# Performance work log

Hardware: AMD Instinct MI355X
Metric: run time of the kernel (lower is better)

## Reference

```python
import jax, jax.numpy as jnp
import numpy as np

B, N, D_IN, D_OUT = 2, 2048, 2048, 2048
H, G = 16, 4            # num_heads, n_kv_groups
HD = D_OUT // H         # head_dim = 128
REP = H // G            # query heads per kv head = 4


def setup_inputs() -> dict:
    key = jax.random.key(0)
    ks = jax.random.split(key, 6)
    s = lambda fan_in: 1.0 / np.sqrt(fan_in)
    return {
        "x": jax.random.normal(ks[0], (B, N, D_IN), jnp.float32),
        "Wq": jax.random.normal(ks[1], (D_IN, D_OUT), jnp.float32) * s(D_IN),
        "Wk": jax.random.normal(ks[2], (D_IN, G * HD), jnp.float32) * s(D_IN),
        "Wv": jax.random.normal(ks[3], (D_IN, G * HD), jnp.float32) * s(D_IN),
        "Wo": jax.random.normal(ks[4], (D_OUT, D_OUT), jnp.float32) * s(D_OUT),
        "bo": jnp.zeros((D_OUT,), jnp.float32),
    }


def reference(x, Wq, Wk, Wv, Wo, bo):
    b, n, _ = x.shape
    # projections
    q = (x @ Wq).reshape(b, n, G, REP, HD)   # query heads grouped: h = g*REP + r
    k = (x @ Wk).reshape(b, n, G, HD)
    v = (x @ Wv).reshape(b, n, G, HD)
    # grouped attention scores; KV broadcast over REP instead of repeat_kv
    scores = jnp.einsum('bqgrd,bkgd->bgrqk', q, k)  # [b,G,REP,N,N]
    causal = jnp.tril(jnp.ones((n, n), bool))       # allowed positions
    scores = jnp.where(causal, scores, -jnp.inf)
    w = jax.nn.softmax(scores / np.float32(np.sqrt(HD)), axis=-1)
    ctx = jnp.einsum('bgrqk,bkgd->bqgrd', w, v).reshape(b, n, D_OUT)
    return ctx @ Wo + bo
```

## Files before the change

kernel.cpp:

```cpp
#include <hip/hip_runtime.h>
#include <stdint.h>

typedef __attribute__((ext_vector_type(8))) __bf16 bf16x8;
typedef __attribute__((ext_vector_type(4))) float f32x4;
typedef __attribute__((ext_vector_type(4))) short short4v;

static constexpr int SEQ  = 2048;
static constexpr int DQKV = 3072;
static constexpr int HD   = 128;

__device__ __forceinline__ short f2bf(float f) {
  unsigned u = __builtin_bit_cast(unsigned, f);
  u += 0x7fffu + ((u >> 16) & 1u);
  return (short)(u >> 16);
}

__device__ __forceinline__ unsigned pack2(float a, float b) {
  return (unsigned)(unsigned short)f2bf(a) | ((unsigned)(unsigned short)f2bf(b) << 16);
}

__device__ __forceinline__ void gl_lds16(const void* g, void* l) {
  __builtin_amdgcn_global_load_lds(
      (const __attribute__((address_space(1))) void*)g,
      (__attribute__((address_space(3))) void*)l, 16, 0, 0);
}

__global__ __launch_bounds__(256)
void prep_kernel(const float* __restrict__ x, const float* __restrict__ Wq,
                 const float* __restrict__ Wk, const float* __restrict__ Wv,
                 const float* __restrict__ Wo,
                 short* __restrict__ xb, short* __restrict__ WqkvT,
                 short* __restrict__ WoT) {
  int blk = blockIdx.x, tid = threadIdx.x;
  if (blk < 8192) {
    int i = blk * 256 + tid;
    float4 v = reinterpret_cast<const float4*>(x)[i];
    short4v o;
    o[0] = f2bf(v.x); o[1] = f2bf(v.y); o[2] = f2bf(v.z); o[3] = f2bf(v.w);
    *reinterpret_cast<short4v*>(xb + (size_t)i * 4) = o;
    return;
  }
  blk -= 8192;
  __shared__ float tile[32][33];
  const float* in; short* out; int C, bx, by;
  if (blk < 4096)      { in = Wq; out = WqkvT;                     C = 2048; bx = blk & 63; by = blk >> 6; }
  else if (blk < 5120) { int t = blk - 4096; in = Wk; out = WqkvT + (size_t)2048 * 2048; C = 512; bx = t & 15; by = t >> 4; }
  else if (blk < 6144) { int t = blk - 5120; in = Wv; out = WqkvT + (size_t)2560 * 2048; C = 512; bx = t & 15; by = t >> 4; }
  else                 { int t = blk - 6144; in = Wo; out = WoT;   C = 2048; bx = t & 63; by = t >> 6; }
  const int R = 2048;
  int c0 = bx * 32, r0 = by * 32, tx = tid & 31, ty = tid >> 5;
  for (int i = 0; i < 4; i++)
    tile[ty + i * 8][tx] = in[(size_t)(r0 + ty + i * 8) * C + c0 + tx];
  __syncthreads();
  for (int i = 0; i < 4; i++)
    out[(size_t)(c0 + ty + i * 8) * R + r0 + tx] = f2bf(tile[tx][ty + i * 8]);
}

template <int MODE>
__device__ __forceinline__
void gemm_body(const short* __restrict__ A, const short* __restrict__ BT,
               void* __restrict__ Cout, const float* __restrict__ bias,
               short* __restrict__ vTout, int N, int K, int GX, float qscale) {
  __shared__ __align__(16) short As[4096];
  __shared__ __align__(16) short Bs[4096];
  const int tid = threadIdx.x, lane = tid & 63, w = tid >> 6;
  const int l15 = lane & 15, quad = lane >> 4, q8 = quad * 8;
  const int bid = blockIdx.x, stripe = GX >> 3;
  const int bx = (bid & 7) * stripe + ((bid >> 3) % stripe);
  const int by = (bid >> 3) / stripe;
  const int row0 = by * 128, col0 = bx * 128;
  const int wm = (w >> 1) * 64, wn = (w & 1) * 64;
  f32x4 acc[4][4] = {};
  const short* ga0 = A  + (size_t)(row0 + w * 16 + (lane >> 2)) * K + (lane & 3) * 8;
  const short* gb0 = BT + (size_t)(col0 + w * 16 + (lane >> 2)) * K + (lane & 3) * 8;
  for (int kt = 0; kt < K; kt += 32) {
    gl_lds16(ga0 + kt,                   As + w * 512);
    gl_lds16(ga0 + (size_t)64 * K + kt,  As + 2048 + w * 512);
    gl_lds16(gb0 + kt,                   Bs + w * 512);
    gl_lds16(gb0 + (size_t)64 * K + kt,  Bs + 2048 + w * 512);
    __syncthreads();
    bf16x8 af[4], bfr[4];
    for (int i = 0; i < 4; i++)
      af[i] = *reinterpret_cast<const bf16x8*>(As + (wm + i * 16 + l15) * 32 + q8);
    for (int j = 0; j < 4; j++)
      bfr[j] = *reinterpret_cast<const bf16x8*>(Bs + (wn + j * 16 + l15) * 32 + q8);
    for (int i = 0; i < 4; i++)
      for (int j = 0; j < 4; j++)
        acc[i][j] = __builtin_amdgcn_mfma_f32_16x16x32_bf16(af[i], bfr[j], acc[i][j], 0, 0, 0);
    __syncthreads();
  }
  if (MODE == 1) {
    float* C = (float*)Cout;
    for (int j = 0; j < 4; j++) {
      int col = col0 + wn + j * 16 + l15;
      float bv = bias[col];
      for (int i = 0; i < 4; i++)
        for (int r = 0; r < 4; r++)
          C[(size_t)(row0 + wm + i * 16 + quad * 4 + r) * N + col] = acc[i][j][r] + bv;
    }
  } else {
    short* C = (short*)Cout;
    for (int j = 0; j < 4; j++) {
      int col = col0 + wn + j * 16 + l15;
      float sc = (col < 2048) ? qscale : 1.0f;
      for (int i = 0; i < 4; i++)
        for (int r = 0; r < 4; r++)
          C[(size_t)(row0 + wm + i * 16 + quad * 4 + r) * N + col] = f2bf(acc[i][j][r] * sc);
    }
    if (col0 >= 2560) {
      for (int j = 0; j < 4; j++) {
        int vc = col0 + wn + j * 16 + l15 - 2560;
        for (int i = 0; i < 4; i++) {
          int rowg = row0 + wm + i * 16 + quad * 4;
          int b = rowg >> 11, n = rowg & 2047;
          uint2 dd = make_uint2(
              (unsigned)(unsigned short)f2bf(acc[i][j][0]) |
                  ((unsigned)(unsigned short)f2bf(acc[i][j][1]) << 16),
              (unsigned)(unsigned short)f2bf(acc[i][j][2]) |
                  ((unsigned)(unsigned short)f2bf(acc[i][j][3]) << 16));
          *reinterpret_cast<uint2*>(vTout + (size_t)(b * 512 + vc) * 2048 + n) = dd;
        }
      }
    }
  }
}

__global__ __launch_bounds__(256)
void qkv_gemm_kernel(const short* __restrict__ A, const short* __restrict__ BT,
                     short* __restrict__ C, short* __restrict__ vT, float qscale) {
  gemm_body<0>(A, BT, C, nullptr, vT, 3072, 2048, 24, qscale);
}

__global__ __launch_bounds__(256)
void out_gemm_kernel(const short* __restrict__ A, const short* __restrict__ BT,
                     float* __restrict__ C, const float* __restrict__ bias) {
  gemm_body<1>(A, BT, C, bias, nullptr, 2048, 2048, 16, 1.0f);
}

__global__ __launch_bounds__(256, 2)
void attn_kernel(const short* __restrict__ qkv, const short* __restrict__ vT,
                 short* __restrict__ ctx) {
  __shared__ __align__(16) short Ks[16384];
  __shared__ __align__(16) short Vs[16384];
  __shared__ __align__(16) short Ps[4608];
  const int tid = threadIdx.x, lane = tid & 63, w = tid >> 6;
  const int l15 = lane & 15, quad = lane >> 4, q8 = quad * 8;
  const int idx = blockIdx.x;
  const int qt = 31 - (idx >> 5);
  const int h = (idx >> 1) & 15, b = idx & 1, g = h >> 2;

  bf16x8 qf[4];
  {
    const short* gq = qkv + (size_t)(b * SEQ + qt * 64 + w * 16 + l15) * DQKV + h * HD + q8;
    for (int ds = 0; ds < 4; ds++)
      qf[ds] = *reinterpret_cast<const bf16x8*>(gq + ds * 32);
  }
  bf16x8 ones;
  for (int i = 0; i < 8; i++) ones[i] = __builtin_bit_cast(__bf16, (short)0x3F80);

  f32x4 acco[8] = {};
  f32x4 accl = {};

  auto stage = [&](int buf, int kt) {
    const short* gk = qkv + (size_t)(b * SEQ + kt * 64 + w * 16 + (lane >> 2)) * DQKV +
                      2048 + g * HD + (lane & 3) * 8;
    for (int ks = 0; ks < 4; ks++)
      gl_lds16(gk + ks * 32, Ks + buf * 8192 + ks * 2048 + w * 512);
    for (int c = 0; c < 2; c++)
      for (int ih = 0; ih < 2; ih++)
        gl_lds16(vT + (size_t)(b * 512 + g * HD + ih * 64 + w * 16 + (lane >> 2)) * SEQ +
                     kt * 64 + c * 32 + (lane & 3) * 8,
                 Vs + buf * 8192 + c * 4096 + ih * 2048 + w * 512);
  };

  stage(0, 0);
  for (int kt = 0; kt <= qt; kt++) {
    const int cur = kt & 1;
    __syncthreads();
    if (kt < qt) stage(cur ^ 1, kt + 1);

    const short* Kb = Ks + cur * 8192;
    const short* Vb = Vs + cur * 8192;

    f32x4 accs[4] = {};
    for (int ds = 0; ds < 4; ds++)
      for (int j = 0; j < 4; j++) {
        bf16x8 kf = *reinterpret_cast<const bf16x8*>(Kb + ds * 2048 + (j * 16 + l15) * 32 + q8);
        accs[j] = __builtin_amdgcn_mfma_f32_16x16x32_bf16(kf, qf[ds], accs[j], 0, 0, 0);
      }

    if (kt == qt) {
      const int q = w * 16 + l15;
      for (int j = 0; j < 4; j++)
        for (int r = 0; r < 4; r++)
          if (j * 16 + quad * 4 + r > q) accs[j][r] = -1e38f;
    }

    for (int j = 0; j < 4; j++) {
      float p0 = exp2f(accs[j][0]), p1 = exp2f(accs[j][1]);
      float p2 = exp2f(accs[j][2]), p3 = exp2f(accs[j][3]);
      unsigned u0 = __builtin_bit_cast(unsigned, p0), u1 = __builtin_bit_cast(unsigned, p1);
      unsigned u2 = __builtin_bit_cast(unsigned, p2), u3 = __builtin_bit_cast(unsigned, p3);
      uint2 dd = make_uint2((u0 >> 16) | (u1 & 0xffff0000u),
                            (u2 >> 16) | (u3 & 0xffff0000u));
      *reinterpret_cast<uint2*>(Ps + w * 1152 + l15 * 72 + j * 16 + quad * 4) = dd;
    }
    asm volatile("s_waitcnt lgkmcnt(0)" ::: "memory");

    for (int c = 0; c < 2; c++) {
      bf16x8 pf = *reinterpret_cast<const bf16x8*>(Ps + w * 1152 + l15 * 72 + c * 32 + q8);
      accl = __builtin_amdgcn_mfma_f32_16x16x32_bf16(ones, pf, accl, 0, 0, 0);
      for (int nt = 0; nt < 8; nt++) {
        bf16x8 vf = *reinterpret_cast<const bf16x8*>(Vb + c * 4096 + (nt * 16 + l15) * 32 + q8);
        acco[nt] = __builtin_amdgcn_mfma_f32_16x16x32_bf16(vf, pf, acco[nt], 0, 0, 0);
      }
    }
  }

  const float invl = 1.f / accl[0];
  const size_t row = (size_t)(b * SEQ + qt * 64 + w * 16 + l15);
  for (int nt = 0; nt < 8; nt++) {
    uint2 dd = make_uint2(pack2(acco[nt][0] * invl, acco[nt][1] * invl),
                          pack2(acco[nt][2] * invl, acco[nt][3] * invl));
    *reinterpret_cast<uint2*>(ctx + row * 2048 + h * HD + nt * 16 + quad * 4) = dd;
  }
}

extern "C" void kernel_launch(void* const* d_in, const int* in_sizes, int n_in,
                              void* d_out, int out_size, void* d_ws, size_t ws_size,
                              hipStream_t stream) {
  const float* x  = (const float*)d_in[0];
  const float* Wq = (const float*)d_in[1];
  const float* Wk = (const float*)d_in[2];
  const float* Wv = (const float*)d_in[3];
  const float* Wo = (const float*)d_in[4];
  const float* bo = (const float*)d_in[5];
  float* out = (float*)d_out;

  const float sc2 = 0.08838834764831845f * 1.4426950408889634f;

  short* xb    = (short*)d_ws;
  short* WqkvT = xb    + (size_t)4096 * 2048;
  short* WoT   = WqkvT + (size_t)3072 * 2048;
  short* qkv   = WoT   + (size_t)2048 * 2048;
  short* vT    = qkv   + (size_t)4096 * 3072;
  short* ctx   = vT    + (size_t)1024 * 2048;

  prep_kernel<<<dim3(18432), dim3(256), 0, stream>>>(x, Wq, Wk, Wv, Wo, xb, WqkvT, WoT);
  qkv_gemm_kernel<<<dim3(768), dim3(256), 0, stream>>>(xb, WqkvT, qkv, vT, sc2);
  attn_kernel<<<dim3(1024), dim3(256), 0, stream>>>(qkv, vT, ctx);
  out_gemm_kernel<<<dim3(512), dim3(256), 0, stream>>>(ctx, WoT, out, bo);
}
```

Before: 314.3 us.

## Split V transpose into separate kernel and use plain 2D GEMM grid

Replaces the swizzled 1D block mapping in the GEMMs with a plain 2D grid and removes the V-transpose write from the QKV GEMM epilogue, adding a standalone tiled transpose kernel instead. This simplifies the GEMM epilogue and removes the strided vT stores from it. In exchange it adds a kernel launch, re-reads V from global memory, and gives up the L2-locality grouping of the previous block order.

After: 305.6 us. 2.8% less time.

```diff
diff --git a/kernel.cpp b/kernel.cpp
--- a/kernel.cpp
+++ b/kernel.cpp
@@ -56,19 +56,28 @@
     out[(size_t)(c0 + ty + i * 8) * R + r0 + tx] = f2bf(tile[tx][ty + i * 8]);
 }
 
-template <int MODE>
-__device__ __forceinline__
-void gemm_body(const short* __restrict__ A, const short* __restrict__ BT,
-               void* __restrict__ Cout, const float* __restrict__ bias,
-               short* __restrict__ vTout, int N, int K, int GX, float qscale) {
+__global__ __launch_bounds__(256) void transpose_v_kernel(const short* __restrict__ qkv,
+                                                          short* __restrict__ vT) {
+  __shared__ short tile[32][33];
+  int n0 = blockIdx.x * 32, c0 = blockIdx.y * 32, b = blockIdx.z;
+  int tx = threadIdx.x & 31, ty = threadIdx.x >> 5;
+  for (int i = 0; i < 4; i++)
+    tile[ty + i * 8][tx] = qkv[(size_t)(b * SEQ + n0 + ty + i * 8) * DQKV + 2560 + c0 + tx];
+  __syncthreads();
+  for (int i = 0; i < 4; i++)
+    vT[(size_t)(b * 512 + c0 + ty + i * 8) * SEQ + n0 + tx] = tile[tx][ty + i * 8];
+}
+
+template <int F32OUT>
+__global__ __launch_bounds__(256)
+void gemm_bt_kernel(const short* __restrict__ A, const short* __restrict__ BT,
+                    void* __restrict__ Cout, const float* __restrict__ bias,
+                    int M, int N, int K, int qcols, float qscale) {
   __shared__ __align__(16) short As[4096];
   __shared__ __align__(16) short Bs[4096];
   const int tid = threadIdx.x, lane = tid & 63, w = tid >> 6;
   const int l15 = lane & 15, quad = lane >> 4, q8 = quad * 8;
-  const int bid = blockIdx.x, stripe = GX >> 3;
-  const int bx = (bid & 7) * stripe + ((bid >> 3) % stripe);
-  const int by = (bid >> 3) / stripe;
-  const int row0 = by * 128, col0 = bx * 128;
+  const int row0 = blockIdx.y * 128, col0 = blockIdx.x * 128;
   const int wm = (w >> 1) * 64, wn = (w & 1) * 64;
   f32x4 acc[4][4] = {};
   const short* ga0 = A  + (size_t)(row0 + w * 16 + (lane >> 2)) * K + (lane & 3) * 8;
@@ -89,7 +98,7 @@
         acc[i][j] = __builtin_amdgcn_mfma_f32_16x16x32_bf16(af[i], bfr[j], acc[i][j], 0, 0, 0);
     __syncthreads();
   }
-  if (MODE == 1) {
+  if (F32OUT) {
     float* C = (float*)Cout;
     for (int j = 0; j < 4; j++) {
       int col = col0 + wn + j * 16 + l15;
@@ -102,39 +111,12 @@
     short* C = (short*)Cout;
     for (int j = 0; j < 4; j++) {
       int col = col0 + wn + j * 16 + l15;
-      float sc = (col < 2048) ? qscale : 1.0f;
+      float sc = (col < qcols) ? qscale : 1.0f;
       for (int i = 0; i < 4; i++)
         for (int r = 0; r < 4; r++)
           C[(size_t)(row0 + wm + i * 16 + quad * 4 + r) * N + col] = f2bf(acc[i][j][r] * sc);
     }
-    if (col0 >= 2560) {
-      for (int j = 0; j < 4; j++) {
-        int vc = col0 + wn + j * 16 + l15 - 2560;
-        for (int i = 0; i < 4; i++) {
-          int rowg = row0 + wm + i * 16 + quad * 4;
-          int b = rowg >> 11, n = rowg & 2047;
-          uint2 dd = make_uint2(
-              (unsigned)(unsigned short)f2bf(acc[i][j][0]) |
-                  ((unsigned)(unsigned short)f2bf(acc[i][j][1]) << 16),
-              (unsigned)(unsigned short)f2bf(acc[i][j][2]) |
-                  ((unsigned)(unsigned short)f2bf(acc[i][j][3]) << 16));
-          *reinterpret_cast<uint2*>(vTout + (size_t)(b * 512 + vc) * 2048 + n) = dd;
-        }
-      }
-    }
-  }
-}
-
-__global__ __launch_bounds__(256)
-void qkv_gemm_kernel(const short* __restrict__ A, const short* __restrict__ BT,
-                     short* __restrict__ C, short* __restrict__ vT, float qscale) {
-  gemm_body<0>(A, BT, C, nullptr, vT, 3072, 2048, 24, qscale);
-}
-
-__global__ __launch_bounds__(256)
-void out_gemm_kernel(const short* __restrict__ A, const short* __restrict__ BT,
-                     float* __restrict__ C, const float* __restrict__ bias) {
-  gemm_body<1>(A, BT, C, bias, nullptr, 2048, 2048, 16, 1.0f);
+  }
 }
 
 __global__ __launch_bounds__(256, 2)
@@ -247,7 +229,10 @@
   short* ctx   = vT    + (size_t)1024 * 2048;
 
   prep_kernel<<<dim3(18432), dim3(256), 0, stream>>>(x, Wq, Wk, Wv, Wo, xb, WqkvT, WoT);
-  qkv_gemm_kernel<<<dim3(768), dim3(256), 0, stream>>>(xb, WqkvT, qkv, vT, sc2);
+  gemm_bt_kernel<0><<<dim3(24, 32), dim3(256), 0, stream>>>(xb, WqkvT, qkv, nullptr,
+                                                            4096, 3072, 2048, 2048, sc2);
+  transpose_v_kernel<<<dim3(64, 16, 2), dim3(256), 0, stream>>>(qkv, vT);
   attn_kernel<<<dim3(1024), dim3(256), 0, stream>>>(qkv, vT, ctx);
-  out_gemm_kernel<<<dim3(512), dim3(256), 0, stream>>>(ctx, WoT, out, bo);
-}
+  gemm_bt_kernel<1><<<dim3(16, 32), dim3(256), 0, stream>>>(ctx, WoT, out, bo,
+                                                            4096, 2048, 2048, 0, 1.0f);
+}
```
